# Kernel optimization log

Hardware: AMD Instinct MI355X
Metric: run time of the kernel (lower is better)

The kernel has to match this reference:

```python
import jax, jax.numpy as jnp
import numpy as np

N_NODES = 50000
N_EDGES = 800000
SIZES = [128, 256, 256, 128]
EPS = 1e-5


def setup_inputs() -> dict:
    key = jax.random.key(0)
    ks = jax.random.split(key, 2 + 5 * (len(SIZES) - 1))
    inp = {
        "x": jax.random.normal(ks[0], (N_NODES, SIZES[0]), dtype=jnp.float32),
        "edge_index": jax.random.randint(ks[1], (2, N_EDGES), 0, N_NODES, dtype=jnp.int64),
    }
    k = 2
    for i, (fin, fout) in enumerate(zip(SIZES[:-1], SIZES[1:])):
        scale = 1.0 / np.sqrt(fin)
        inp[f"W{i}"] = jax.random.normal(ks[k], (fout, fin), dtype=jnp.float32) * scale; k += 1
        inp[f"b{i}"] = jnp.zeros((fout,), dtype=jnp.float32)
        inp[f"g{i}"] = jnp.ones((fout,), dtype=jnp.float32)   # LayerNorm weight
        inp[f"be{i}"] = jnp.zeros((fout,), dtype=jnp.float32)  # LayerNorm bias
        inp[f"a{i}"] = jnp.full((1,), 0.25, dtype=jnp.float32)  # PReLU slope
        k += 3  # keep key consumption deterministic
    return inp


def _gcn_conv(x, src, dst, dinv, W, b):
    # GCNConv: h = x @ W^T; aggregate norm(src,dst) * h[src] into dst; add bias.
    h = x @ W.T  # [N, F_out]
    norm = dinv[src] * dinv[dst]  # [E+N]
    msg = norm[:, None] * h[src]  # [E+N, F_out]
    return jax.ops.segment_sum(msg, dst, num_segments=N_NODES) + b


def _layernorm_graph(x, g, be):
    # PyG LayerNorm(mode='graph'): normalize over all nodes and channels.
    mu = x.mean()
    xc = x - mu
    var = (xc * xc).mean()
    return xc / jnp.sqrt(var + EPS) * g + be


def _prelu(x, a):
    return jnp.where(x >= 0, x, a * x)


def reference(x, edge_index, W0, b0, g0, be0, a0, W1, b1, g1, be1, a1, W2, b2, g2, be2, a2):
    loop = jnp.arange(N_NODES, dtype=edge_index.dtype)
    src = jnp.concatenate([edge_index[0], loop])  # add self-loops
    dst = jnp.concatenate([edge_index[1], loop])
    deg = jax.ops.segment_sum(jnp.ones_like(dst, dtype=x.dtype), dst, num_segments=N_NODES)
    dinv = jax.lax.rsqrt(deg)  # deg >= 1 due to self-loops
    params = [(W0, b0, g0, be0, a0), (W1, b1, g1, be1, a1), (W2, b2, g2, be2, a2)]
    for W, b, g, be, a in params:
        x = _gcn_conv(x, src, dst, dinv, W, b)
        x = _layernorm_graph(x, g, be)
        x = _prelu(x, a)
    return x
```

## Files before the change

### kernel.cpp

```cpp
#include <hip/hip_runtime.h>

#define N_NODES 50000
#define N_EDGES 800000
#define EPS 1e-5f

typedef __attribute__((ext_vector_type(8))) short bf16x8;
typedef __attribute__((ext_vector_type(4))) float f32x4;
typedef __attribute__((ext_vector_type(4))) unsigned short us4;

__device__ __forceinline__ unsigned short f2b(float f) {
    union { float f; unsigned int u; } v; v.f = f;
    unsigned int r = v.u + 0x7fffu + ((v.u >> 16) & 1u);
    return (unsigned short)(r >> 16);
}
__device__ __forceinline__ float b2f(unsigned short b) {
    union { unsigned int u; float f; } v; v.u = ((unsigned int)b) << 16;
    return v.f;
}

#define RED_FLOATS_PER_LAYER 1024


__global__ void init_kernel(int* __restrict__ deg, int* __restrict__ fill,
                            float* __restrict__ red, int n) {
    int i = blockIdx.x * blockDim.x + threadIdx.x;
    if (i < n) { deg[i] = 0; fill[i] = 0; }
    if (i < 3 * RED_FLOATS_PER_LAYER) red[i] = 0.f;
}

__global__ void count_kernel(const int* __restrict__ dst, int* __restrict__ deg, int e) {
    for (int i = blockIdx.x * blockDim.x + threadIdx.x; i < e; i += gridDim.x * blockDim.x)
        atomicAdd(&deg[dst[i]], 1);
}

__global__ void dinv_kernel(const int* __restrict__ deg, float* __restrict__ dinv, int n) {
    int i = blockIdx.x * blockDim.x + threadIdx.x;
    if (i < n) dinv[i] = rsqrtf((float)(deg[i] + 1));
}

__global__ void scan1_kernel(const int* __restrict__ deg, int* __restrict__ bsum, int n) {
    int i = blockIdx.x * 256 + threadIdx.x;
    int v = (i < n) ? deg[i] : 0;
    #pragma unroll
    for (int off = 1; off < 64; off <<= 1) v += __shfl_xor(v, off);
    __shared__ int wsum[4];
    int wid = threadIdx.x >> 6, lane = threadIdx.x & 63;
    if (lane == 0) wsum[wid] = v;
    __syncthreads();
    if (threadIdx.x == 0) bsum[blockIdx.x] = wsum[0] + wsum[1] + wsum[2] + wsum[3];
}

__global__ void scan2_kernel(const int* __restrict__ bsum, int* __restrict__ bpre, int nb) {
    __shared__ int sm[256];
    int t = threadIdx.x;
    sm[t] = (t < nb) ? bsum[t] : 0;
    __syncthreads();
    #pragma unroll
    for (int d = 1; d < 256; d <<= 1) {
        int x = (t >= d) ? sm[t - d] : 0;
        __syncthreads();
        sm[t] += x;
        __syncthreads();
    }
    bpre[t] = (t > 0) ? sm[t - 1] : 0;
}

__global__ void scan3_kernel(const int* __restrict__ deg, const int* __restrict__ bpre,
                             int* __restrict__ off, int n) {
    __shared__ int sm[256];
    int t = threadIdx.x;
    int i = blockIdx.x * 256 + t;
    int v = (i < n) ? deg[i] : 0;
    sm[t] = v;
    __syncthreads();
    #pragma unroll
    for (int d = 1; d < 256; d <<= 1) {
        int x = (t >= d) ? sm[t - d] : 0;
        __syncthreads();
        sm[t] += x;
        __syncthreads();
    }
    if (i < n) off[i + 1] = sm[t] + bpre[blockIdx.x];
    if (i == 0) off[0] = 0;
}

__global__ void scatter_kernel(const int* __restrict__ src, const int* __restrict__ dst,
                               const int* __restrict__ coff, int* __restrict__ fill,
                               const float* __restrict__ dinv,
                               int* __restrict__ csrc, float* __restrict__ cw, int e) {
    for (int i = blockIdx.x * blockDim.x + threadIdx.x; i < e; i += gridDim.x * blockDim.x) {
        int d = dst[i];
        int s = src[i];
        int pos = coff[d] + atomicAdd(&fill[d], 1);
        csrc[pos] = s;
        cw[pos] = dinv[s] * dinv[d];
    }
}


__global__ void convert_kernel(const float* __restrict__ src, unsigned short* __restrict__ dst,
                               int n4) {
    int i = blockIdx.x * blockDim.x + threadIdx.x;
    if (i < n4) {
        float4 v = reinterpret_cast<const float4*>(src)[i];
        us4 o;
        o[0] = f2b(v.x); o[1] = f2b(v.y); o[2] = f2b(v.z); o[3] = f2b(v.w);
        reinterpret_cast<us4*>(dst)[i] = o;
    }
}


template<int BN, bool TRANSFORM, bool ADD_BIAS, bool FUSE_RED, bool OUT_BF16>
__global__ __launch_bounds__(256) void gemm_fused(
    const void* __restrict__ Xin, const unsigned short* __restrict__ Wb,
    const float* __restrict__ bias, const float* __restrict__ redin,
    const float* __restrict__ gw, const float* __restrict__ bw,
    const float* __restrict__ asl, float* __restrict__ redout,
    void* __restrict__ Hout, int M, int K, float inv_count) {
    constexpr int FR_N = BN / 64;
    __shared__ unsigned short xs[64 * 32];
    __shared__ unsigned short wsm[BN * 32];
    int m0 = blockIdx.x * 64;
    int tid = threadIdx.x;
    int wid = tid >> 6, lane = tid & 63;
    int l16 = lane & 15, kg = lane >> 4;
    int srow = tid >> 2, sblk = tid & 3;

    float mu = 0.f, rstd = 0.f, alpha = 0.f;
    if (TRANSFORM) {
        float s = redin[lane * 16], s2 = redin[lane * 16 + 1];
        #pragma unroll
        for (int off = 1; off < 64; off <<= 1) { s += __shfl_xor(s, off); s2 += __shfl_xor(s2, off); }
        mu = s * inv_count;
        rstd = rsqrtf(s2 * inv_count - mu * mu + EPS);
        alpha = asl[0];
    }

    f32x4 acc[4][FR_N] = {};
    for (int k0 = 0; k0 < K; k0 += 32) {
        int gm = m0 + srow;
        bf16x8 xv = {};
        if (TRANSFORM) {
            if (gm < M) {
                const float* xp = (const float*)Xin + (size_t)gm * K + k0 + sblk * 8;
                float4 u0 = *(const float4*)xp;
                float4 u1 = *(const float4*)(xp + 4);
                float t[8] = {u0.x, u0.y, u0.z, u0.w, u1.x, u1.y, u1.z, u1.w};
                #pragma unroll
                for (int i = 0; i < 8; ++i) {
                    int f = k0 + sblk * 8 + i;
                    float v = (t[i] - mu) * rstd * gw[f] + bw[f];
                    v = v >= 0.f ? v : alpha * v;
                    xv[i] = (short)f2b(v);
                }
            }
        } else {
            if (gm < M)
                xv = *reinterpret_cast<const bf16x8*>((const unsigned short*)Xin +
                                                      (size_t)gm * K + k0 + sblk * 8);
        }
        *reinterpret_cast<bf16x8*>(xs + srow * 32 + ((sblk ^ (srow & 3)) * 8)) = xv;
        #pragma unroll
        for (int i = 0; i < BN / 64; ++i) {
            int idx = tid + i * 256;
            int wrow = idx >> 2, wblk = idx & 3;
            bf16x8 wv = *reinterpret_cast<const bf16x8*>(Wb + (size_t)wrow * K + k0 + wblk * 8);
            *reinterpret_cast<bf16x8*>(wsm + wrow * 32 + ((wblk ^ (wrow & 3)) * 8)) = wv;
        }
        __syncthreads();
        bf16x8 a[4], b[FR_N];
        #pragma unroll
        for (int f = 0; f < 4; ++f) {
            int ar = f * 16 + l16;
            a[f] = *reinterpret_cast<const bf16x8*>(xs + ar * 32 + ((kg ^ (ar & 3)) * 8));
        }
        #pragma unroll
        for (int f = 0; f < FR_N; ++f) {
            int br = wid * (FR_N * 16) + f * 16 + l16;
            b[f] = *reinterpret_cast<const bf16x8*>(wsm + br * 32 + ((kg ^ (br & 3)) * 8));
        }
        #pragma unroll
        for (int i = 0; i < 4; ++i)
            #pragma unroll
            for (int j = 0; j < FR_N; ++j)
                acc[i][j] = __builtin_amdgcn_mfma_f32_16x16x32_bf16(a[i], b[j], acc[i][j], 0, 0, 0);
        __syncthreads();
    }

    float s = 0.f, s2 = 0.f;
    #pragma unroll
    for (int i = 0; i < 4; ++i) {
        #pragma unroll
        for (int j = 0; j < FR_N; ++j) {
            int col = wid * (FR_N * 16) + j * 16 + l16;
            float bv = ADD_BIAS ? bias[col] : 0.f;
            #pragma unroll
            for (int r = 0; r < 4; ++r) {
                int row = m0 + i * 16 + kg * 4 + r;
                if (row < M) {
                    float v = acc[i][j][r] + bv;
                    if (FUSE_RED) { s += v; s2 += v * v; }
                    if (OUT_BF16)
                        ((unsigned short*)Hout)[(size_t)row * BN + col] = f2b(v);
                    else
                        ((float*)Hout)[(size_t)row * BN + col] = v;
                }
            }
        }
    }
    if (FUSE_RED) {
        #pragma unroll
        for (int off = 1; off < 64; off <<= 1) { s += __shfl_xor(s, off); s2 += __shfl_xor(s2, off); }
        if (lane == 0) {
            int bkt = (blockIdx.x & 63) * 16;
            atomicAdd(&redout[bkt], s);
            atomicAdd(&redout[bkt + 1], s2);
        }
    }
}


template<int COLS, bool ADD_BIAS, bool OUT_BF16, bool FUSE_RED>
__global__ void aggregate2(const unsigned short* __restrict__ Hb,
                           const int* __restrict__ coff, const int* __restrict__ csrc,
                           const float* __restrict__ cw, const float* __restrict__ dinv,
                           const float* __restrict__ bias, void* __restrict__ Y,
                           float* __restrict__ red) {
    constexpr int RL = COLS / 8;
    constexpr int NG = 64 / RL;
    int node = blockIdx.x * 4 + (threadIdx.x >> 6);
    if (node >= N_NODES) return;
    int lane = threadIdx.x & 63;
    int g = lane / RL;
    int rl = lane % RL;
    float di = dinv[node];
    int s0 = coff[node], s1 = coff[node + 1];
    float acc[8] = {};
    for (int k = s0 - 1 + g; k < s1; k += NG) {
        int s; float w;
        if (k < s0) { s = node; w = di * di; }
        else { s = csrc[k]; w = cw[k]; }
        bf16x8 v = *reinterpret_cast<const bf16x8*>(Hb + (size_t)s * COLS + rl * 8);
        #pragma unroll
        for (int i = 0; i < 8; ++i) acc[i] += w * b2f((unsigned short)v[i]);
    }
    #pragma unroll
    for (int off = RL; off < 64; off <<= 1) {
        #pragma unroll
        for (int i = 0; i < 8; ++i) acc[i] += __shfl_xor(acc[i], off);
    }
    if (ADD_BIAS) {
        #pragma unroll
        for (int i = 0; i < 8; ++i) acc[i] += bias[rl * 8 + i];
    }
    if (FUSE_RED) {
        float s = 0.f, s2 = 0.f;
        if (g == 0) {
            #pragma unroll
            for (int i = 0; i < 8; ++i) { s += acc[i]; s2 += acc[i] * acc[i]; }
        }
        #pragma unroll
        for (int off = 1; off < 64; off <<= 1) { s += __shfl_xor(s, off); s2 += __shfl_xor(s2, off); }
        if (lane == 0) {
            int bkt = (blockIdx.x & 63) * 16;
            atomicAdd(&red[bkt], s);
            atomicAdd(&red[bkt + 1], s2);
        }
    }
    if (g == 0) {
        if (OUT_BF16) {
            bf16x8 o;
            #pragma unroll
            for (int i = 0; i < 8; ++i) o[i] = (short)f2b(acc[i]);
            *reinterpret_cast<bf16x8*>((unsigned short*)Y + (size_t)node * COLS + rl * 8) = o;
        } else {
            float* yp = (float*)Y + (size_t)node * COLS + rl * 8;
            *reinterpret_cast<float4*>(yp) = make_float4(acc[0], acc[1], acc[2], acc[3]);
            *reinterpret_cast<float4*>(yp + 4) = make_float4(acc[4], acc[5], acc[6], acc[7]);
        }
    }
}


__global__ void norm_final(const float* __restrict__ Y, const float* __restrict__ red,
                           const float* __restrict__ g, const float* __restrict__ be,
                           const float* __restrict__ a, float* __restrict__ X,
                           int fmask4, int n4, float inv_count) {
    int lane = threadIdx.x & 63;
    float s = red[lane * 16], s2 = red[lane * 16 + 1];
    #pragma unroll
    for (int off = 1; off < 64; off <<= 1) { s += __shfl_xor(s, off); s2 += __shfl_xor(s2, off); }
    float mu = s * inv_count;
    float rstd = rsqrtf(s2 * inv_count - mu * mu + EPS);
    float alpha = a[0];
    for (int i = blockIdx.x * blockDim.x + threadIdx.x; i < n4; i += gridDim.x * blockDim.x) {
        float4 v = reinterpret_cast<const float4*>(Y)[i];
        int f4 = (i & fmask4) * 4;
        float o[4] = {v.x, v.y, v.z, v.w};
        #pragma unroll
        for (int j = 0; j < 4; ++j) {
            float t = (o[j] - mu) * rstd * g[f4 + j] + be[f4 + j];
            o[j] = t >= 0.f ? t : alpha * t;
        }
        reinterpret_cast<float4*>(X)[i] = make_float4(o[0], o[1], o[2], o[3]);
    }
}


extern "C" void kernel_launch(void* const* d_in, const int* in_sizes, int n_in,
                              void* d_out, int out_size, void* d_ws, size_t ws_size,
                              hipStream_t stream) {
    const float* x0 = (const float*)d_in[0];
    const int* ei = (const int*)d_in[1];
    const float* W[3] = {(const float*)d_in[2], (const float*)d_in[7], (const float*)d_in[12]};
    const float* bb[3] = {(const float*)d_in[3], (const float*)d_in[8], (const float*)d_in[13]};
    const float* gg[3] = {(const float*)d_in[4], (const float*)d_in[9], (const float*)d_in[14]};
    const float* be[3] = {(const float*)d_in[5], (const float*)d_in[10], (const float*)d_in[15]};
    const float* aa[3] = {(const float*)d_in[6], (const float*)d_in[11], (const float*)d_in[16]};

    char* ws = (char*)d_ws;
    size_t o = 0;
    auto alloc = [&](size_t bytes) {
        void* p = ws + o;
        o = (o + bytes + 255) & ~(size_t)255;
        return p;
    };
    int* deg = (int*)alloc(N_NODES * 4);
    int* fill = (int*)alloc(N_NODES * 4);
    int* coff = (int*)alloc((N_NODES + 1) * 4);
    int* csrc = (int*)alloc(N_EDGES * 4);
    float* cw = (float*)alloc(N_EDGES * 4);
    float* dinv = (float*)alloc(N_NODES * 4);
    int* bsum = (int*)alloc(256 * 4);
    int* bpre = (int*)alloc(256 * 4);
    float* red = (float*)alloc(3 * RED_FLOATS_PER_LAYER * 4);
    unsigned short* Wb0 = (unsigned short*)alloc(256 * 128 * 2);
    unsigned short* Wb1 = (unsigned short*)alloc(256 * 256 * 2);
    unsigned short* Wb2 = (unsigned short*)alloc(128 * 256 * 2);
    unsigned short* xb = (unsigned short*)alloc((size_t)N_NODES * 128 * 2);
    unsigned short* hb = (unsigned short*)alloc((size_t)N_NODES * 256 * 2);
    float* y = (float*)alloc((size_t)N_NODES * 256 * 4);

    const int* e_src = ei;
    const int* e_dst = ei + N_EDGES;
    int nb = (N_NODES + 255) / 256;

    init_kernel<<<(N_NODES + 255) / 256, 256, 0, stream>>>(deg, fill, red, N_NODES);
    count_kernel<<<1024, 256, 0, stream>>>(e_dst, deg, N_EDGES);
    dinv_kernel<<<(N_NODES + 255) / 256, 256, 0, stream>>>(deg, dinv, N_NODES);
    scan1_kernel<<<nb, 256, 0, stream>>>(deg, bsum, N_NODES);
    scan2_kernel<<<1, 256, 0, stream>>>(bsum, bpre, nb);
    scan3_kernel<<<nb, 256, 0, stream>>>(deg, bpre, coff, N_NODES);
    scatter_kernel<<<1024, 256, 0, stream>>>(e_src, e_dst, coff, fill, dinv, csrc, cw, N_EDGES);

    convert_kernel<<<(N_NODES * 128 / 4 + 255) / 256, 256, 0, stream>>>(x0, xb, N_NODES * 128 / 4);
    convert_kernel<<<(256 * 128 / 4 + 255) / 256, 256, 0, stream>>>(W[0], Wb0, 256 * 128 / 4);
    convert_kernel<<<(256 * 256 / 4 + 255) / 256, 256, 0, stream>>>(W[1], Wb1, 256 * 256 / 4);
    convert_kernel<<<(128 * 256 / 4 + 255) / 256, 256, 0, stream>>>(W[2], Wb2, 128 * 256 / 4);

    int gm = (N_NODES + 63) / 64;

    aggregate2<128, false, true, false><<<12500, 256, 0, stream>>>(xb, coff, csrc, cw, dinv,
                                                                   nullptr, hb, nullptr);
    gemm_fused<256, false, true, true, false><<<gm, 256, 0, stream>>>(
        hb, Wb0, bb[0], nullptr, nullptr, nullptr, nullptr, red + 0, y, N_NODES, 128,
        1.0f / (N_NODES * 256.0f));

    gemm_fused<256, true, false, false, true><<<gm, 256, 0, stream>>>(
        y, Wb1, nullptr, red + 0, gg[0], be[0], aa[0], nullptr, hb, N_NODES, 256,
        1.0f / (N_NODES * 256.0f));
    aggregate2<256, true, false, true><<<12500, 256, 0, stream>>>(
        hb, coff, csrc, cw, dinv, bb[1], y, red + RED_FLOATS_PER_LAYER);

    gemm_fused<128, true, false, false, true><<<gm, 256, 0, stream>>>(
        y, Wb2, nullptr, red + RED_FLOATS_PER_LAYER, gg[1], be[1], aa[1], nullptr, hb,
        N_NODES, 256, 1.0f / (N_NODES * 256.0f));
    aggregate2<128, true, false, true><<<12500, 256, 0, stream>>>(
        hb, coff, csrc, cw, dinv, bb[2], y, red + 2 * RED_FLOATS_PER_LAYER);

    norm_final<<<2048, 256, 0, stream>>>(y, red + 2 * RED_FLOATS_PER_LAYER, gg[2], be[2], aa[2],
                                         (float*)d_out, 31, N_NODES * 128 / 4,
                                         1.0f / (N_NODES * 128.0f));
}
```

Before: 360.2 us.

## Split aggregation by column chunks and spread edges across sixteen lane groups

The sparse aggregation kernel now gives each wavefront one 32-column chunk of a node instead of the whole row. Each chunk has 16 lane groups walking the node's edges in parallel, where before there were 2 to 4 groups. This adds more blocks and more memory requests in flight, aiming at the latency of gathering neighbour rows. The reduction buckets for the graph LayerNorm statistics grow from 64 to 512 to ease atomic contention from the larger grid, and readers now sum more buckets. The cost is that the CSR offsets, sources and weights are re-read once per column chunk.

```diff
diff --git a/kernel.cpp b/kernel.cpp
--- a/kernel.cpp
+++ b/kernel.cpp
@@ -18,7 +18,8 @@
     return v.f;
 }
 
-#define RED_FLOATS_PER_LAYER 1024
+#define RED_BUCKETS 512
+#define RED_FLOATS_PER_LAYER (RED_BUCKETS * 16)
 
 
 __global__ void init_kernel(int* __restrict__ deg, int* __restrict__ fill,
@@ -128,7 +129,12 @@
 
     float mu = 0.f, rstd = 0.f, alpha = 0.f;
     if (TRANSFORM) {
-        float s = redin[lane * 16], s2 = redin[lane * 16 + 1];
+        float s = 0.f, s2 = 0.f;
+        #pragma unroll
+        for (int j = 0; j < RED_BUCKETS / 64; ++j) {
+            s += redin[(lane + j * 64) * 16];
+            s2 += redin[(lane + j * 64) * 16 + 1];
+        }
         #pragma unroll
         for (int off = 1; off < 64; off <<= 1) { s += __shfl_xor(s, off); s2 += __shfl_xor(s2, off); }
         mu = s * inv_count;
@@ -212,7 +218,7 @@
         #pragma unroll
         for (int off = 1; off < 64; off <<= 1) { s += __shfl_xor(s, off); s2 += __shfl_xor(s2, off); }
         if (lane == 0) {
-            int bkt = (blockIdx.x & 63) * 16;
+            int bkt = (blockIdx.x % RED_BUCKETS) * 16;
             atomicAdd(&redout[bkt], s);
             atomicAdd(&redout[bkt + 1], s2);
         }
@@ -221,37 +227,38 @@
 
 
 template<int COLS, bool ADD_BIAS, bool OUT_BF16, bool FUSE_RED>
-__global__ void aggregate2(const unsigned short* __restrict__ Hb,
+__global__ void aggregate3(const unsigned short* __restrict__ Hb,
                            const int* __restrict__ coff, const int* __restrict__ csrc,
                            const float* __restrict__ cw, const float* __restrict__ dinv,
                            const float* __restrict__ bias, void* __restrict__ Y,
                            float* __restrict__ red) {
-    constexpr int RL = COLS / 8;
-    constexpr int NG = 64 / RL;
-    int node = blockIdx.x * 4 + (threadIdx.x >> 6);
-    if (node >= N_NODES) return;
+    constexpr int CHUNKS = COLS / 32;
+    int chunk = blockIdx.x % CHUNKS;
+    int nblk = blockIdx.x / CHUNKS;
+    int node = nblk * 4 + (threadIdx.x >> 6);
     int lane = threadIdx.x & 63;
-    int g = lane / RL;
-    int rl = lane % RL;
+    int g = lane >> 2;
+    int rl = lane & 3;
+    int c0 = chunk * 32 + rl * 8;
     float di = dinv[node];
     int s0 = coff[node], s1 = coff[node + 1];
     float acc[8] = {};
-    for (int k = s0 - 1 + g; k < s1; k += NG) {
+    for (int k = s0 - 1 + g; k < s1; k += 16) {
         int s; float w;
         if (k < s0) { s = node; w = di * di; }
         else { s = csrc[k]; w = cw[k]; }
-        bf16x8 v = *reinterpret_cast<const bf16x8*>(Hb + (size_t)s * COLS + rl * 8);
+        bf16x8 v = *reinterpret_cast<const bf16x8*>(Hb + (size_t)s * COLS + c0);
         #pragma unroll
         for (int i = 0; i < 8; ++i) acc[i] += w * b2f((unsigned short)v[i]);
     }
     #pragma unroll
-    for (int off = RL; off < 64; off <<= 1) {
+    for (int off = 4; off < 64; off <<= 1) {
         #pragma unroll
         for (int i = 0; i < 8; ++i) acc[i] += __shfl_xor(acc[i], off);
     }
     if (ADD_BIAS) {
         #pragma unroll
-        for (int i = 0; i < 8; ++i) acc[i] += bias[rl * 8 + i];
+        for (int i = 0; i < 8; ++i) acc[i] += bias[c0 + i];
     }
     if (FUSE_RED) {
         float s = 0.f, s2 = 0.f;
@@ -262,7 +269,7 @@
         #pragma unroll
         for (int off = 1; off < 64; off <<= 1) { s += __shfl_xor(s, off); s2 += __shfl_xor(s2, off); }
         if (lane == 0) {
-            int bkt = (blockIdx.x & 63) * 16;
+            int bkt = (blockIdx.x % RED_BUCKETS) * 16;
             atomicAdd(&red[bkt], s);
             atomicAdd(&red[bkt + 1], s2);
         }
@@ -272,9 +279,9 @@
             bf16x8 o;
             #pragma unroll
             for (int i = 0; i < 8; ++i) o[i] = (short)f2b(acc[i]);
-            *reinterpret_cast<bf16x8*>((unsigned short*)Y + (size_t)node * COLS + rl * 8) = o;
+            *reinterpret_cast<bf16x8*>((unsigned short*)Y + (size_t)node * COLS + c0) = o;
         } else {
-            float* yp = (float*)Y + (size_t)node * COLS + rl * 8;
+            float* yp = (float*)Y + (size_t)node * COLS + c0;
             *reinterpret_cast<float4*>(yp) = make_float4(acc[0], acc[1], acc[2], acc[3]);
             *reinterpret_cast<float4*>(yp + 4) = make_float4(acc[4], acc[5], acc[6], acc[7]);
         }
@@ -287,7 +294,12 @@
                            const float* __restrict__ a, float* __restrict__ X,
                            int fmask4, int n4, float inv_count) {
     int lane = threadIdx.x & 63;
-    float s = red[lane * 16], s2 = red[lane * 16 + 1];
+    float s = 0.f, s2 = 0.f;
+    #pragma unroll
+    for (int j = 0; j < RED_BUCKETS / 64; ++j) {
+        s += red[(lane + j * 64) * 16];
+        s2 += red[(lane + j * 64) * 16 + 1];
+    }
     #pragma unroll
     for (int off = 1; off < 64; off <<= 1) { s += __shfl_xor(s, off); s2 += __shfl_xor(s2, off); }
     float mu = s * inv_count;
@@ -360,8 +372,8 @@
 
     int gm = (N_NODES + 63) / 64;
 
-    aggregate2<128, false, true, false><<<12500, 256, 0, stream>>>(xb, coff, csrc, cw, dinv,
-                                                                   nullptr, hb, nullptr);
+    aggregate3<128, false, true, false><<<12500 * 4, 256, 0, stream>>>(
+        xb, coff, csrc, cw, dinv, nullptr, hb, nullptr);
     gemm_fused<256, false, true, true, false><<<gm, 256, 0, stream>>>(
         hb, Wb0, bb[0], nullptr, nullptr, nullptr, nullptr, red + 0, y, N_NODES, 128,
         1.0f / (N_NODES * 256.0f));
@@ -369,13 +381,13 @@
     gemm_fused<256, true, false, false, true><<<gm, 256, 0, stream>>>(
         y, Wb1, nullptr, red + 0, gg[0], be[0], aa[0], nullptr, hb, N_NODES, 256,
         1.0f / (N_NODES * 256.0f));
-    aggregate2<256, true, false, true><<<12500, 256, 0, stream>>>(
+    aggregate3<256, true, false, true><<<12500 * 8, 256, 0, stream>>>(
         hb, coff, csrc, cw, dinv, bb[1], y, red + RED_FLOATS_PER_LAYER);
 
     gemm_fused<128, true, false, false, true><<<gm, 256, 0, stream>>>(
         y, Wb2, nullptr, red + RED_FLOATS_PER_LAYER, gg[1], be[1], aa[1], nullptr, hb,
         N_NODES, 256, 1.0f / (N_NODES * 256.0f));
-    aggregate2<128, true, false, true><<<12500, 256, 0, stream>>>(
+    aggregate3<128, true, false, true><<<12500 * 4, 256, 0, stream>>>(
         hb, coff, csrc, cw, dinv, bb[2], y, red + 2 * RED_FLOATS_PER_LAYER);
 
     norm_final<<<2048, 256, 0, stream>>>(y, red + 2 * RED_FLOATS_PER_LAYER, gg[2], be[2], aa[2],
```

After: 552.0 us. +53.3%, slower.

## Store intermediate activations in bf16 and merge small setup kernels

Applied to the files above, without the earlier changes.

Pre-normalization activations between stages are now stored as bf16 instead of fp32. This roughly halves the global traffic for the intermediate buffer written by GEMM/aggregate and read by the next GEMM and the final norm. The dinv computation is folded into scan1, and the four conversion launches are merged into one. This cuts launch count, and count/scatter grid sizes are doubled. The risk is extra rounding error before LayerNorm, and the removed node bounds check in aggregate2 assumes an exact grid.

```diff
diff --git a/kernel.cpp b/kernel.cpp
--- a/kernel.cpp
+++ b/kernel.cpp
@@ -18,7 +18,8 @@
     return v.f;
 }
 
-#define RED_FLOATS_PER_LAYER 1024
+#define RED_BUCKETS 64
+#define RED_FLOATS_PER_LAYER (RED_BUCKETS * 16)
 
 
 __global__ void init_kernel(int* __restrict__ deg, int* __restrict__ fill,
@@ -33,19 +34,17 @@
         atomicAdd(&deg[dst[i]], 1);
 }
 
-__global__ void dinv_kernel(const int* __restrict__ deg, float* __restrict__ dinv, int n) {
-    int i = blockIdx.x * blockDim.x + threadIdx.x;
-    if (i < n) dinv[i] = rsqrtf((float)(deg[i] + 1));
-}
-
-__global__ void scan1_kernel(const int* __restrict__ deg, int* __restrict__ bsum, int n) {
+__global__ void scan1_kernel(const int* __restrict__ deg, float* __restrict__ dinv,
+                             int* __restrict__ bsum, int n) {
     int i = blockIdx.x * 256 + threadIdx.x;
     int v = (i < n) ? deg[i] : 0;
-    #pragma unroll
-    for (int off = 1; off < 64; off <<= 1) v += __shfl_xor(v, off);
+    if (i < n) dinv[i] = rsqrtf((float)(v + 1));
+    int t = v;
+    #pragma unroll
+    for (int off = 1; off < 64; off <<= 1) t += __shfl_xor(t, off);
     __shared__ int wsum[4];
     int wid = threadIdx.x >> 6, lane = threadIdx.x & 63;
-    if (lane == 0) wsum[wid] = v;
+    if (lane == 0) wsum[wid] = t;
     __syncthreads();
     if (threadIdx.x == 0) bsum[blockIdx.x] = wsum[0] + wsum[1] + wsum[2] + wsum[3];
 }
@@ -98,25 +97,38 @@
 }
 
 
-__global__ void convert_kernel(const float* __restrict__ src, unsigned short* __restrict__ dst,
-                               int n4) {
-    int i = blockIdx.x * blockDim.x + threadIdx.x;
-    if (i < n4) {
-        float4 v = reinterpret_cast<const float4*>(src)[i];
-        us4 o;
-        o[0] = f2b(v.x); o[1] = f2b(v.y); o[2] = f2b(v.z); o[3] = f2b(v.w);
-        reinterpret_cast<us4*>(dst)[i] = o;
-    }
-}
-
-
-template<int BN, bool TRANSFORM, bool ADD_BIAS, bool FUSE_RED, bool OUT_BF16>
+#define CV_NX (N_NODES * 128 / 4)
+#define CV_N0 (256 * 128 / 4)
+#define CV_N1 (256 * 256 / 4)
+#define CV_N2 (128 * 256 / 4)
+
+__global__ void convert_all(const float* __restrict__ x0, const float* __restrict__ W0,
+                            const float* __restrict__ W1, const float* __restrict__ W2,
+                            unsigned short* __restrict__ xb, unsigned short* __restrict__ wb0,
+                            unsigned short* __restrict__ wb1, unsigned short* __restrict__ wb2) {
+    int i = blockIdx.x * 256 + threadIdx.x;
+    const float* s;
+    unsigned short* d;
+    int j = i;
+    if (j < CV_NX) { s = x0; d = xb; }
+    else if ((j -= CV_NX) < CV_N0) { s = W0; d = wb0; }
+    else if ((j -= CV_N0) < CV_N1) { s = W1; d = wb1; }
+    else if ((j -= CV_N1) < CV_N2) { s = W2; d = wb2; }
+    else return;
+    float4 v = reinterpret_cast<const float4*>(s)[j];
+    us4 o;
+    o[0] = f2b(v.x); o[1] = f2b(v.y); o[2] = f2b(v.z); o[3] = f2b(v.w);
+    reinterpret_cast<us4*>(d)[j] = o;
+}
+
+
+template<int BN, bool TRANSFORM, bool ADD_BIAS, bool FUSE_RED>
 __global__ __launch_bounds__(256) void gemm_fused(
-    const void* __restrict__ Xin, const unsigned short* __restrict__ Wb,
+    const unsigned short* __restrict__ Xin, const unsigned short* __restrict__ Wb,
     const float* __restrict__ bias, const float* __restrict__ redin,
     const float* __restrict__ gw, const float* __restrict__ bw,
     const float* __restrict__ asl, float* __restrict__ redout,
-    void* __restrict__ Hout, int M, int K, float inv_count) {
+    unsigned short* __restrict__ Hout, int M, int K, float inv_count) {
     constexpr int FR_N = BN / 64;
     __shared__ unsigned short xs[64 * 32];
     __shared__ unsigned short wsm[BN * 32];
@@ -140,24 +152,19 @@
     for (int k0 = 0; k0 < K; k0 += 32) {
         int gm = m0 + srow;
         bf16x8 xv = {};
-        if (TRANSFORM) {
-            if (gm < M) {
-                const float* xp = (const float*)Xin + (size_t)gm * K + k0 + sblk * 8;
-                float4 u0 = *(const float4*)xp;
-                float4 u1 = *(const float4*)(xp + 4);
-                float t[8] = {u0.x, u0.y, u0.z, u0.w, u1.x, u1.y, u1.z, u1.w};
+        if (gm < M) {
+            bf16x8 u = *reinterpret_cast<const bf16x8*>(Xin + (size_t)gm * K + k0 + sblk * 8);
+            if (TRANSFORM) {
                 #pragma unroll
                 for (int i = 0; i < 8; ++i) {
                     int f = k0 + sblk * 8 + i;
-                    float v = (t[i] - mu) * rstd * gw[f] + bw[f];
+                    float v = (b2f((unsigned short)u[i]) - mu) * rstd * gw[f] + bw[f];
                     v = v >= 0.f ? v : alpha * v;
                     xv[i] = (short)f2b(v);
                 }
+            } else {
+                xv = u;
             }
-        } else {
-            if (gm < M)
-                xv = *reinterpret_cast<const bf16x8*>((const unsigned short*)Xin +
-                                                      (size_t)gm * K + k0 + sblk * 8);
         }
         *reinterpret_cast<bf16x8*>(xs + srow * 32 + ((sblk ^ (srow & 3)) * 8)) = xv;
         #pragma unroll
@@ -200,10 +207,7 @@
                 if (row < M) {
                     float v = acc[i][j][r] + bv;
                     if (FUSE_RED) { s += v; s2 += v * v; }
-                    if (OUT_BF16)
-                        ((unsigned short*)Hout)[(size_t)row * BN + col] = f2b(v);
-                    else
-                        ((float*)Hout)[(size_t)row * BN + col] = v;
+                    Hout[(size_t)row * BN + col] = f2b(v);
                 }
             }
         }
@@ -212,7 +216,7 @@
         #pragma unroll
         for (int off = 1; off < 64; off <<= 1) { s += __shfl_xor(s, off); s2 += __shfl_xor(s2, off); }
         if (lane == 0) {
-            int bkt = (blockIdx.x & 63) * 16;
+            int bkt = (blockIdx.x & (RED_BUCKETS - 1)) * 16;
             atomicAdd(&redout[bkt], s);
             atomicAdd(&redout[bkt + 1], s2);
         }
@@ -220,16 +224,15 @@
 }
 
 
-template<int COLS, bool ADD_BIAS, bool OUT_BF16, bool FUSE_RED>
+template<int COLS, bool ADD_BIAS, bool FUSE_RED>
 __global__ void aggregate2(const unsigned short* __restrict__ Hb,
                            const int* __restrict__ coff, const int* __restrict__ csrc,
                            const float* __restrict__ cw, const float* __restrict__ dinv,
-                           const float* __restrict__ bias, void* __restrict__ Y,
+                           const float* __restrict__ bias, unsigned short* __restrict__ Y,
                            float* __restrict__ red) {
     constexpr int RL = COLS / 8;
     constexpr int NG = 64 / RL;
     int node = blockIdx.x * 4 + (threadIdx.x >> 6);
-    if (node >= N_NODES) return;
     int lane = threadIdx.x & 63;
     int g = lane / RL;
     int rl = lane % RL;
@@ -262,30 +265,24 @@
         #pragma unroll
         for (int off = 1; off < 64; off <<= 1) { s += __shfl_xor(s, off); s2 += __shfl_xor(s2, off); }
         if (lane == 0) {
-            int bkt = (blockIdx.x & 63) * 16;
+            int bkt = (blockIdx.x & (RED_BUCKETS - 1)) * 16;
             atomicAdd(&red[bkt], s);
             atomicAdd(&red[bkt + 1], s2);
         }
     }
     if (g == 0) {
-        if (OUT_BF16) {
-            bf16x8 o;
-            #pragma unroll
-            for (int i = 0; i < 8; ++i) o[i] = (short)f2b(acc[i]);
-            *reinterpret_cast<bf16x8*>((unsigned short*)Y + (size_t)node * COLS + rl * 8) = o;
-        } else {
-            float* yp = (float*)Y + (size_t)node * COLS + rl * 8;
-            *reinterpret_cast<float4*>(yp) = make_float4(acc[0], acc[1], acc[2], acc[3]);
-            *reinterpret_cast<float4*>(yp + 4) = make_float4(acc[4], acc[5], acc[6], acc[7]);
-        }
-    }
-}
-
-
-__global__ void norm_final(const float* __restrict__ Y, const float* __restrict__ red,
+        bf16x8 o;
+        #pragma unroll
+        for (int i = 0; i < 8; ++i) o[i] = (short)f2b(acc[i]);
+        *reinterpret_cast<bf16x8*>(Y + (size_t)node * COLS + rl * 8) = o;
+    }
+}
+
+
+__global__ void norm_final(const unsigned short* __restrict__ Yb, const float* __restrict__ red,
                            const float* __restrict__ g, const float* __restrict__ be,
                            const float* __restrict__ a, float* __restrict__ X,
-                           int fmask4, int n4, float inv_count) {
+                           int fmask8, int n8, float inv_count) {
     int lane = threadIdx.x & 63;
     float s = red[lane * 16], s2 = red[lane * 16 + 1];
     #pragma unroll
@@ -293,16 +290,18 @@
     float mu = s * inv_count;
     float rstd = rsqrtf(s2 * inv_count - mu * mu + EPS);
     float alpha = a[0];
-    for (int i = blockIdx.x * blockDim.x + threadIdx.x; i < n4; i += gridDim.x * blockDim.x) {
-        float4 v = reinterpret_cast<const float4*>(Y)[i];
-        int f4 = (i & fmask4) * 4;
-        float o[4] = {v.x, v.y, v.z, v.w};
-        #pragma unroll
-        for (int j = 0; j < 4; ++j) {
-            float t = (o[j] - mu) * rstd * g[f4 + j] + be[f4 + j];
+    for (int i = blockIdx.x * blockDim.x + threadIdx.x; i < n8; i += gridDim.x * blockDim.x) {
+        bf16x8 v = reinterpret_cast<const bf16x8*>(Yb)[i];
+        int fb = (i & fmask8) * 8;
+        float o[8];
+        #pragma unroll
+        for (int j = 0; j < 8; ++j) {
+            float t = (b2f((unsigned short)v[j]) - mu) * rstd * g[fb + j] + be[fb + j];
             o[j] = t >= 0.f ? t : alpha * t;
         }
-        reinterpret_cast<float4*>(X)[i] = make_float4(o[0], o[1], o[2], o[3]);
+        float* xp = X + (size_t)i * 8;
+        *reinterpret_cast<float4*>(xp) = make_float4(o[0], o[1], o[2], o[3]);
+        *reinterpret_cast<float4*>(xp + 4) = make_float4(o[4], o[5], o[6], o[7]);
     }
 }
 
@@ -339,46 +338,43 @@
     unsigned short* Wb2 = (unsigned short*)alloc(128 * 256 * 2);
     unsigned short* xb = (unsigned short*)alloc((size_t)N_NODES * 128 * 2);
     unsigned short* hb = (unsigned short*)alloc((size_t)N_NODES * 256 * 2);
-    float* y = (float*)alloc((size_t)N_NODES * 256 * 4);
+    unsigned short* yb = (unsigned short*)alloc((size_t)N_NODES * 256 * 2);
 
     const int* e_src = ei;
     const int* e_dst = ei + N_EDGES;
     int nb = (N_NODES + 255) / 256;
 
     init_kernel<<<(N_NODES + 255) / 256, 256, 0, stream>>>(deg, fill, red, N_NODES);
-    count_kernel<<<1024, 256, 0, stream>>>(e_dst, deg, N_EDGES);
-    dinv_kernel<<<(N_NODES + 255) / 256, 256, 0, stream>>>(deg, dinv, N_NODES);
-    scan1_kernel<<<nb, 256, 0, stream>>>(deg, bsum, N_NODES);
+    count_kernel<<<2048, 256, 0, stream>>>(e_dst, deg, N_EDGES);
+    scan1_kernel<<<nb, 256, 0, stream>>>(deg, dinv, bsum, N_NODES);
     scan2_kernel<<<1, 256, 0, stream>>>(bsum, bpre, nb);
     scan3_kernel<<<nb, 256, 0, stream>>>(deg, bpre, coff, N_NODES);
-    scatter_kernel<<<1024, 256, 0, stream>>>(e_src, e_dst, coff, fill, dinv, csrc, cw, N_EDGES);
-
-    convert_kernel<<<(N_NODES * 128 / 4 + 255) / 256, 256, 0, stream>>>(x0, xb, N_NODES * 128 / 4);
-    convert_kernel<<<(256 * 128 / 4 + 255) / 256, 256, 0, stream>>>(W[0], Wb0, 256 * 128 / 4);
-    convert_kernel<<<(256 * 256 / 4 + 255) / 256, 256, 0, stream>>>(W[1], Wb1, 256 * 256 / 4);
-    convert_kernel<<<(128 * 256 / 4 + 255) / 256, 256, 0, stream>>>(W[2], Wb2, 128 * 256 / 4);
+    scatter_kernel<<<2048, 256, 0, stream>>>(e_src, e_dst, coff, fill, dinv, csrc, cw, N_EDGES);
+
+    int cvtot = CV_NX + CV_N0 + CV_N1 + CV_N2;
+    convert_all<<<(cvtot + 255) / 256, 256, 0, stream>>>(x0, W[0], W[1], W[2], xb, Wb0, Wb1, Wb2);
 
     int gm = (N_NODES + 63) / 64;
 
-    aggregate2<128, false, true, false><<<12500, 256, 0, stream>>>(xb, coff, csrc, cw, dinv,
-                                                                   nullptr, hb, nullptr);
-    gemm_fused<256, false, true, true, false><<<gm, 256, 0, stream>>>(
-        hb, Wb0, bb[0], nullptr, nullptr, nullptr, nullptr, red + 0, y, N_NODES, 128,
+    aggregate2<128, false, false><<<12500, 256, 0, stream>>>(xb, coff, csrc, cw, dinv,
+                                                             nullptr, hb, nullptr);
+    gemm_fused<256, false, true, true><<<gm, 256, 0, stream>>>(
+        hb, Wb0, bb[0], nullptr, nullptr, nullptr, nullptr, red + 0, yb, N_NODES, 128,
         1.0f / (N_NODES * 256.0f));
 
-    gemm_fused<256, true, false, false, true><<<gm, 256, 0, stream>>>(
-        y, Wb1, nullptr, red + 0, gg[0], be[0], aa[0], nullptr, hb, N_NODES, 256,
+    gemm_fused<256, true, false, false><<<gm, 256, 0, stream>>>(
+        yb, Wb1, nullptr, red + 0, gg[0], be[0], aa[0], nullptr, hb, N_NODES, 256,
         1.0f / (N_NODES * 256.0f));
-    aggregate2<256, true, false, true><<<12500, 256, 0, stream>>>(
-        hb, coff, csrc, cw, dinv, bb[1], y, red + RED_FLOATS_PER_LAYER);
-
-    gemm_fused<128, true, false, false, true><<<gm, 256, 0, stream>>>(
-        y, Wb2, nullptr, red + RED_FLOATS_PER_LAYER, gg[1], be[1], aa[1], nullptr, hb,
+    aggregate2<256, true, true><<<12500, 256, 0, stream>>>(
+        hb, coff, csrc, cw, dinv, bb[1], yb, red + RED_FLOATS_PER_LAYER);
+
+    gemm_fused<128, true, false, false><<<gm, 256, 0, stream>>>(
+        yb, Wb2, nullptr, red + RED_FLOATS_PER_LAYER, gg[1], be[1], aa[1], nullptr, hb,
         N_NODES, 256, 1.0f / (N_NODES * 256.0f));
-    aggregate2<128, true, false, true><<<12500, 256, 0, stream>>>(
-        hb, coff, csrc, cw, dinv, bb[2], y, red + 2 * RED_FLOATS_PER_LAYER);
-
-    norm_final<<<2048, 256, 0, stream>>>(y, red + 2 * RED_FLOATS_PER_LAYER, gg[2], be[2], aa[2],
-                                         (float*)d_out, 31, N_NODES * 128 / 4,
+    aggregate2<128, true, true><<<12500, 256, 0, stream>>>(
+        hb, coff, csrc, cw, dinv, bb[2], yb, red + 2 * RED_FLOATS_PER_LAYER);
+
+    norm_final<<<2048, 256, 0, stream>>>(yb, red + 2 * RED_FLOATS_PER_LAYER, gg[2], be[2], aa[2],
+                                         (float*)d_out, 15, N_NODES * 128 / 8,
                                          1.0f / (N_NODES * 128.0f));
 }
```

Measured after the change: 339.9 us. 5.6% less time.
